# Kernel optimization log

Measured on AMD Instinct MI355X. Metric: run time of the kernel, lower is better.

The kernel has to match this reference:

```python
import math
import jax, jax.numpy as jnp
import numpy as np
from jax import lax

B, S, D, H, L, F, V = 4, 2048, 768, 12, 6, 3072, 512
HD = D // H
EPS = 1e-5


def setup_inputs():
    key = jax.random.key(0)
    ks = jax.random.split(key, 18)
    std = 0.02
    inp = {
        'x': jax.random.randint(ks[0], (B, S), 0, V, dtype=jnp.int64)
            if jax.config.jax_enable_x64 else jax.random.randint(ks[0], (B, S), 0, V, dtype=jnp.int32),
        'emb': jax.random.normal(ks[1], (V, D), jnp.float32) * std,
        'qkv_w': jax.random.normal(ks[2], (L, D, 3 * D), jnp.float32) * std,
        'qkv_b': jnp.zeros((L, 3 * D), jnp.float32),
        'out_w': jax.random.normal(ks[3], (L, D, D), jnp.float32) * std,
        'out_b': jnp.zeros((L, D), jnp.float32),
        'ln1_s': jnp.ones((L, D), jnp.float32),
        'ln1_b': jnp.zeros((L, D), jnp.float32),
        'w1': jax.random.normal(ks[4], (L, D, F), jnp.float32) * std,
        'b1': jnp.zeros((L, F), jnp.float32),
        'w2': jax.random.normal(ks[5], (L, F, D), jnp.float32) * std,
        'b2': jnp.zeros((L, D), jnp.float32),
        'ln2_s': jnp.ones((L, D), jnp.float32),
        'ln2_b': jnp.zeros((L, D), jnp.float32),
        'lnf_s': jnp.ones((D,), jnp.float32),
        'lnf_b': jnp.zeros((D,), jnp.float32),
        'head_w': jax.random.normal(ks[6], (D, V), jnp.float32) * std,
        'head_b': jnp.zeros((V,), jnp.float32),
    }
    return inp


def _layer_norm(x, s, b):
    mu = jnp.mean(x, -1, keepdims=True)
    var = jnp.mean(jnp.square(x - mu), -1, keepdims=True)
    return (x - mu) * lax.rsqrt(var + EPS) * s + b


def _pos_encoding(seq_len, d_model, dtype):
    pos = jnp.arange(seq_len, dtype=dtype)[:, None]
    div = jnp.exp(jnp.arange(0, d_model, 2, dtype=dtype) * (-math.log(10000.0) / d_model))
    pe = jnp.zeros((seq_len, d_model), dtype)
    pe = pe.at[:, 0::2].set(jnp.sin(pos * div))
    pe = pe.at[:, 1::2].set(jnp.cos(pos * div))
    return pe


def reference(x, emb, qkv_w, qkv_b, out_w, out_b, ln1_s, ln1_b,
              w1, b1, w2, b2, ln2_s, ln2_b, lnf_s, lnf_b, head_w, head_b):
    b, s = x.shape
    d = emb.shape[1]
    h = emb[x] * math.sqrt(d)                      # [B,S,D]
    h = h + _pos_encoding(s, d, h.dtype)
    causal = jnp.tril(jnp.ones((s, s), bool))      # [S,S]
    scale = HD ** -0.5

    def block(hcarry, p):
        qw, qb, ow, ob, l1s, l1b, w1i, b1i, w2i, b2i, l2s, l2b = p
        xn = _layer_norm(hcarry, l1s, l1b)
        qkv = xn @ qw + qb                          # [B,S,3D]
        qkv = qkv.reshape(b, s, 3, H, HD).transpose(2, 0, 3, 1, 4)
        q, k, v = qkv[0], qkv[1], qkv[2]            # each [B,H,S,hd]
        scores = jnp.einsum('bhqd,bhkd->bhqk', q, k) * scale
        scores = jnp.where(causal, scores, -jnp.inf)
        attn = jax.nn.softmax(scores, axis=-1)
        o = jnp.einsum('bhqk,bhkd->bhqd', attn, v)
        o = o.transpose(0, 2, 1, 3).reshape(b, s, d)
        hcarry = hcarry + (o @ ow + ob)
        xn2 = _layer_norm(hcarry, l2s, l2b)
        ff = jax.nn.relu(xn2 @ w1i + b1i) @ w2i + b2i
        return hcarry + ff, None

    h, _ = lax.scan(block, h, (qkv_w, qkv_b, out_w, out_b, ln1_s, ln1_b,
                               w1, b1, w2, b2, ln2_s, ln2_b))
    h = _layer_norm(h, lnf_s, lnf_b)
    return h @ head_w + head_b                     # [B,S,V]
```

## Files before the change

kernel.cpp:

```cpp
#include <hip/hip_runtime.h>
#include <math.h>
#include <stdio.h>

#define Bv 4
#define Sv 2048
#define Dv 768
#define Hv 12
#define Lv 6
#define Fv 3072
#define Vv 512
#define Mv (Bv*Sv)

typedef __bf16 bf16;
typedef __bf16 bf16x8 __attribute__((ext_vector_type(8)));
typedef __bf16 bf16x4 __attribute__((ext_vector_type(4)));
typedef short  s16x4  __attribute__((ext_vector_type(4)));
typedef float  f32x4  __attribute__((ext_vector_type(4)));

__device__ __forceinline__ void gload_lds16(const void* g, void* l) {
  __builtin_amdgcn_global_load_lds(
      (__attribute__((address_space(1))) void*)(void*)g,
      (__attribute__((address_space(3))) void*)l, 16, 0, 0);
}

__device__ __forceinline__ int xcd_remap(int orig, int nwg) {
  int q = nwg >> 3, r = nwg & 7;
  int xcd = orig & 7, loc = orig >> 3;
  return (xcd < r ? xcd * (q + 1) : r * (q + 1) + (xcd - r) * q) + loc;
}

__global__ void detect_i64(const int* __restrict__ x, int* __restrict__ flag) {
  __shared__ int red[256];
  int acc = 0;
  for (int i = threadIdx.x; i < Mv / 2; i += 256) acc |= x[2 * i + 1];
  red[threadIdx.x] = acc;
  __syncthreads();
  for (int s = 128; s > 0; s >>= 1) {
    if (threadIdx.x < s) red[threadIdx.x] |= red[threadIdx.x + s];
    __syncthreads();
  }
  if (threadIdx.x == 0) *flag = (red[0] == 0) ? 1 : 0;
}

__global__ void embed_kernel(const int* __restrict__ x, const float* __restrict__ emb,
                             float* __restrict__ h, const int* __restrict__ i64flag) {
  int idx = blockIdx.x * 256 + threadIdx.x;
  int j  = idx % (Dv / 2);
  int bs = idx / (Dv / 2);
  int s  = bs % Sv;
  int tok = (*i64flag) ? x[2 * bs] : x[bs];
  float2 e = *(const float2*)(emb + (size_t)tok * Dv + 2 * j);
  float div = expf((float)(2 * j) * (-9.210340371976184f / (float)Dv));
  float arg = (float)s * div;
  const float sq = 27.712812921102035f;
  float2 o;
  o.x = e.x * sq + sinf(arg);
  o.y = e.y * sq + cosf(arg);
  *(float2*)(h + (size_t)bs * Dv + 2 * j) = o;
}

__global__ void transpose_cvt(const float* __restrict__ in, bf16* __restrict__ out,
                              int K, int N) {
  __shared__ float tile[64][65];
  in  += (size_t)blockIdx.z * K * N;
  out += (size_t)blockIdx.z * K * N;
  int n0 = blockIdx.x * 64, k0 = blockIdx.y * 64;
  int tx = threadIdx.x & 63, ty = threadIdx.x >> 6;
#pragma unroll
  for (int i = 0; i < 64; i += 4)
    tile[ty + i][tx] = in[(size_t)(k0 + ty + i) * N + n0 + tx];
  __syncthreads();
#pragma unroll
  for (int i = 0; i < 64; i += 4)
    out[(size_t)(n0 + ty + i) * K + k0 + tx] = (bf16)tile[tx][ty + i];
}

__global__ void vtrans(const bf16* __restrict__ qkv, bf16* __restrict__ vt) {
  __shared__ bf16 tile[64][72];
  const int st = blockIdx.x;
  const int bh = blockIdx.y;
  const int b = bh / Hv, h = bh % Hv;
  const bf16* src = qkv + ((size_t)b * Sv + st * 64) * 2304 + 1536 + h * 64;
  const int rl = threadIdx.x >> 3;
  const int c8 = (threadIdx.x & 7) * 8;
#pragma unroll
  for (int i = 0; i < 2; ++i) {
    bf16x8 v = *(const bf16x8*)(src + (size_t)(rl + i * 32) * 2304 + c8);
    *(bf16x8*)&tile[rl + i * 32][c8] = v;
  }
  __syncthreads();
  bf16* dst = vt + ((size_t)bh * 64) * Sv + st * 64;
#pragma unroll
  for (int i = 0; i < 2; ++i) {
    bf16 tmp[8];
#pragma unroll
    for (int j = 0; j < 8; ++j) tmp[j] = tile[c8 + j][rl + i * 32];
    *(bf16x8*)(dst + (size_t)(rl + i * 32) * Sv + c8) = *(bf16x8*)tmp;
  }
}

__global__ void ln_kernel(const float* __restrict__ hin, const float* __restrict__ sc,
                          const float* __restrict__ bi, bf16* __restrict__ out) {
  int row  = blockIdx.x * 4 + (threadIdx.x >> 6);
  int lane = threadIdx.x & 63;
  const float* p = hin + (size_t)row * Dv + lane * 12;
  float v[12];
  *(float4*)(v)     = *(const float4*)(p);
  *(float4*)(v + 4) = *(const float4*)(p + 4);
  *(float4*)(v + 8) = *(const float4*)(p + 8);
  float sum = 0.f, sq = 0.f;
#pragma unroll
  for (int j = 0; j < 12; ++j) { sum += v[j]; sq += v[j] * v[j]; }
#pragma unroll
  for (int m = 1; m < 64; m <<= 1) {
    sum += __shfl_xor(sum, m, 64);
    sq  += __shfl_xor(sq,  m, 64);
  }
  float mu  = sum * (1.f / 768.f);
  float var = sq * (1.f / 768.f) - mu * mu;
  float rs  = rsqrtf(var + 1e-5f);
  float s_[12], b_[12];
  const float* scp = sc + lane * 12;
  const float* bip = bi + lane * 12;
  *(float4*)(s_)     = *(const float4*)(scp);
  *(float4*)(s_ + 4) = *(const float4*)(scp + 4);
  *(float4*)(s_ + 8) = *(const float4*)(scp + 8);
  *(float4*)(b_)     = *(const float4*)(bip);
  *(float4*)(b_ + 4) = *(const float4*)(bip + 4);
  *(float4*)(b_ + 8) = *(const float4*)(bip + 8);
  union { bf16 h2[12]; uint2 q[3]; } ob;
#pragma unroll
  for (int j = 0; j < 12; ++j)
    ob.h2[j] = (bf16)((v[j] - mu) * rs * s_[j] + b_[j]);
  uint2* op = (uint2*)(out + (size_t)row * Dv + lane * 12);
  op[0] = ob.q[0]; op[1] = ob.q[1]; op[2] = ob.q[2];
}

template<bool RELU, bool RESID, int OUTMODE>
__global__ __launch_bounds__(256) void gemm_bt(
    const bf16* __restrict__ A, const bf16* __restrict__ Bt,
    const float* __restrict__ bias, float* __restrict__ hres,
    bf16* __restrict__ outb, float* __restrict__ outf, int M, int N, int K) {
  __shared__ bf16 sA[2][128 * 64];
  __shared__ bf16 sB[2][128 * 64];
  const int gx = gridDim.x;
  const int wg = xcd_remap(blockIdx.y * gx + blockIdx.x, gx * gridDim.y);
  const int bn = (wg % gx) * 128, bm = (wg / gx) * 128;
  const int t = threadIdx.x, lane = t & 63, wid = t >> 6;
  const int wr = wid >> 1, wc = wid & 1;
  const int g = lane >> 4, c = lane & 15;
  f32x4 acc[4][4];
#pragma unroll
  for (int i = 0; i < 4; ++i)
#pragma unroll
    for (int j = 0; j < 4; ++j) acc[i][j] = (f32x4){0.f, 0.f, 0.f, 0.f};
  const int nkt = K >> 6;

  auto stage = [&](int bb, int kt) {
#pragma unroll
    for (int j2 = 0; j2 < 4; ++j2) {
      int ch  = t + j2 * 256;
      int row = ch >> 3;
      int src = ((ch & 7) * 8) ^ ((row & 7) << 3);
      gload_lds16(A  + (size_t)(bm + row) * K + kt * 64 + src, &sA[bb][ch * 8]);
      gload_lds16(Bt + (size_t)(bn + row) * K + kt * 64 + src, &sB[bb][ch * 8]);
    }
  };

  stage(0, 0);
  const int swz = (c & 7) << 3;
  for (int kt = 0; kt < nkt; ++kt) {
    const int cb = kt & 1;
    if (kt + 1 < nkt) {
      stage(cb ^ 1, kt + 1);
      asm volatile("s_waitcnt vmcnt(8)" ::: "memory");
    } else {
      asm volatile("s_waitcnt vmcnt(0)" ::: "memory");
    }
    __builtin_amdgcn_s_barrier();
    __builtin_amdgcn_sched_barrier(0);
#pragma unroll
    for (int f = 0; f < 2; ++f) {
      bf16x8 aF[4], bF[4];
      const int e = (f * 32 + g * 8) ^ swz;
#pragma unroll
      for (int mt = 0; mt < 4; ++mt)
        aF[mt] = *(const bf16x8*)&sA[cb][(wr * 64 + mt * 16 + c) * 64 + e];
#pragma unroll
      for (int nt = 0; nt < 4; ++nt)
        bF[nt] = *(const bf16x8*)&sB[cb][(wc * 64 + nt * 16 + c) * 64 + e];
      __builtin_amdgcn_s_setprio(1);
#pragma unroll
      for (int mt = 0; mt < 4; ++mt)
#pragma unroll
        for (int nt = 0; nt < 4; ++nt)
          acc[mt][nt] = __builtin_amdgcn_mfma_f32_16x16x32_bf16(
              aF[mt], bF[nt], acc[mt][nt], 0, 0, 0);
      __builtin_amdgcn_s_setprio(0);
    }
    __builtin_amdgcn_sched_barrier(0);
    __builtin_amdgcn_s_barrier();
  }
#pragma unroll
  for (int nt = 0; nt < 4; ++nt) {
    int col = bn + wc * 64 + nt * 16 + c;
    float bv = bias[col];
#pragma unroll
    for (int mt = 0; mt < 4; ++mt) {
      int row0 = bm + wr * 64 + mt * 16 + g * 4;
#pragma unroll
      for (int r = 0; r < 4; ++r) {
        float vv = acc[mt][nt][r] + bv;
        if (RELU) vv = fmaxf(vv, 0.f);
        size_t off = (size_t)(row0 + r) * N + col;
        if (RESID) { vv += hres[off]; hres[off] = vv; }
        if (OUTMODE == 1) outb[off] = (bf16)vv;
        if (OUTMODE == 2) outf[off] = vv;
      }
    }
  }
}

template<bool RELU, bool RESID, int OUTMODE>
__global__ __launch_bounds__(256) void gemm_sk(
    const bf16* __restrict__ A, const bf16* __restrict__ Bt,
    const float* __restrict__ bias, float* __restrict__ hres,
    bf16* __restrict__ outb, float* __restrict__ outf, int M, int N, int K) {
  __shared__ bf16 sA[2][64 * 64];
  __shared__ bf16 sB[2][128 * 64];
  const int gx = gridDim.x;
  const int wg = xcd_remap(blockIdx.y * gx + blockIdx.x, gx * gridDim.y);
  const int bn = (wg % gx) * 128, bm = (wg / gx) * 64;
  const int t = threadIdx.x, lane = t & 63, wid = t >> 6;
  const int wr = wid >> 1, wc = wid & 1;
  const int g = lane >> 4, c = lane & 15;
  f32x4 acc[2][4];
#pragma unroll
  for (int i = 0; i < 2; ++i)
#pragma unroll
    for (int j = 0; j < 4; ++j) acc[i][j] = (f32x4){0.f, 0.f, 0.f, 0.f};
  const int nkt = K >> 6;

  auto stage = [&](int bb, int kt) {
#pragma unroll
    for (int j2 = 0; j2 < 2; ++j2) {
      int ch  = t + j2 * 256;
      int row = ch >> 3;
      int src = ((ch & 7) * 8) ^ ((row & 7) << 3);
      gload_lds16(A + (size_t)(bm + row) * K + kt * 64 + src, &sA[bb][ch * 8]);
    }
#pragma unroll
    for (int j2 = 0; j2 < 4; ++j2) {
      int ch  = t + j2 * 256;
      int row = ch >> 3;
      int src = ((ch & 7) * 8) ^ ((row & 7) << 3);
      gload_lds16(Bt + (size_t)(bn + row) * K + kt * 64 + src, &sB[bb][ch * 8]);
    }
  };

  stage(0, 0);
  const int swz = (c & 7) << 3;
  for (int kt = 0; kt < nkt; ++kt) {
    const int cb = kt & 1;
    if (kt + 1 < nkt) {
      stage(cb ^ 1, kt + 1);
      asm volatile("s_waitcnt vmcnt(6)" ::: "memory");
    } else {
      asm volatile("s_waitcnt vmcnt(0)" ::: "memory");
    }
    __builtin_amdgcn_s_barrier();
    __builtin_amdgcn_sched_barrier(0);
#pragma unroll
    for (int f = 0; f < 2; ++f) {
      bf16x8 aF[2], bF[4];
      const int e = (f * 32 + g * 8) ^ swz;
#pragma unroll
      for (int mt = 0; mt < 2; ++mt)
        aF[mt] = *(const bf16x8*)&sA[cb][(wr * 32 + mt * 16 + c) * 64 + e];
#pragma unroll
      for (int nt = 0; nt < 4; ++nt)
        bF[nt] = *(const bf16x8*)&sB[cb][(wc * 64 + nt * 16 + c) * 64 + e];
      __builtin_amdgcn_s_setprio(1);
#pragma unroll
      for (int mt = 0; mt < 2; ++mt)
#pragma unroll
        for (int nt = 0; nt < 4; ++nt)
          acc[mt][nt] = __builtin_amdgcn_mfma_f32_16x16x32_bf16(
              aF[mt], bF[nt], acc[mt][nt], 0, 0, 0);
      __builtin_amdgcn_s_setprio(0);
    }
    __builtin_amdgcn_sched_barrier(0);
    __builtin_amdgcn_s_barrier();
  }
#pragma unroll
  for (int nt = 0; nt < 4; ++nt) {
    int col = bn + wc * 64 + nt * 16 + c;
    float bv = bias[col];
#pragma unroll
    for (int mt = 0; mt < 2; ++mt) {
      int row0 = bm + wr * 32 + mt * 16 + g * 4;
#pragma unroll
      for (int r = 0; r < 4; ++r) {
        float vv = acc[mt][nt][r] + bv;
        if (RELU) vv = fmaxf(vv, 0.f);
        size_t off = (size_t)(row0 + r) * N + col;
        if (RESID) { vv += hres[off]; hres[off] = vv; }
        if (OUTMODE == 1) outb[off] = (bf16)vv;
        if (OUTMODE == 2) outf[off] = vv;
      }
    }
  }
}

__global__ __launch_bounds__(256) void attn_kernel(const bf16* __restrict__ qkv,
                                                   const bf16* __restrict__ vt,
                                                   bf16* __restrict__ o) {
  __shared__ bf16 sK[2][64 * 64], sVT[2][64 * 64];
  const int nwg = 16 * Bv * Hv;
  const int wgl = xcd_remap(blockIdx.y * 16 + blockIdx.x, nwg);
  const int i  = wgl % 16;
  const int bh = wgl / 16;
  const int qtA = i, qtB = 31 - i;
  const int b  = bh / Hv;
  const int h  = bh % Hv;
  const int t = threadIdx.x, lane = t & 63, wid = t >> 6;
  const int g = lane >> 4, c = lane & 15;
  const int QST = 2304;
  const bf16* qbase  = qkv + (size_t)b * Sv * QST + h * 64;
  const bf16* vtbase = vt + ((size_t)bh * 64) * Sv;
  const float CS = 0.18033688011112042f;
  const float THR = 11.541560327111707f;
  const int swz = (c & 7) << 3;
  const s16x4 onesf = {0x3F80, 0x3F80, 0x3F80, 0x3F80};

  bf16x8 qfA[2], qfB[2];
  {
    const bf16* qa = qbase + (size_t)(qtA * 64 + wid * 16 + c) * QST;
    qfA[0] = *(const bf16x8*)(qa + g * 8);
    qfA[1] = *(const bf16x8*)(qa + 32 + g * 8);
    const bf16* qb = qbase + (size_t)(qtB * 64 + wid * 16 + c) * QST;
    qfB[0] = *(const bf16x8*)(qb + g * 8);
    qfB[1] = *(const bf16x8*)(qb + 32 + g * 8);
  }
  f32x4 accA[4], accB[4];
  f32x4 accLA = {0.f, 0.f, 0.f, 0.f}, accLB = {0.f, 0.f, 0.f, 0.f};
  float mA = -INFINITY, mB = -INFINITY;
#pragma unroll
  for (int d0 = 0; d0 < 4; ++d0) {
    accA[d0] = (f32x4){0.f, 0.f, 0.f, 0.f};
    accB[d0] = (f32x4){0.f, 0.f, 0.f, 0.f};
  }
  const int qlA = qtA * 64 + wid * 16 + c;
  const int qlB = qtB * 64 + wid * 16 + c;

  auto stage = [&](int bb, int kt) {
#pragma unroll
    for (int j2 = 0; j2 < 2; ++j2) {
      int ch  = t + j2 * 256;
      int row = ch >> 3;
      int src = ((ch & 7) * 8) ^ ((row & 7) << 3);
      gload_lds16(qbase + (size_t)(kt * 64 + row) * QST + 768 + src, &sK[bb][ch * 8]);
      gload_lds16(vtbase + (size_t)row * Sv + kt * 64 + src, &sVT[bb][ch * 8]);
    }
  };

  auto process = [&](int bb, const bf16x8* qf, f32x4* accO, f32x4& accL,
                     float& m_s, int ql, int kt, bool diag) {
    f32x4 accT[4];
#pragma unroll
    for (int nt = 0; nt < 4; ++nt) accT[nt] = (f32x4){0.f, 0.f, 0.f, 0.f};
    __builtin_amdgcn_s_setprio(1);
#pragma unroll
    for (int nt = 0; nt < 4; ++nt)
#pragma unroll
      for (int f = 0; f < 2; ++f) {
        bf16x8 kf = *(const bf16x8*)&sK[bb][(nt * 16 + c) * 64 + ((f * 32 + g * 8) ^ swz)];
        accT[nt] = __builtin_amdgcn_mfma_f32_16x16x32_bf16(kf, qf[f], accT[nt], 0, 0, 0);
      }
    __builtin_amdgcn_s_setprio(0);
    if (diag) {
#pragma unroll
      for (int nt = 0; nt < 4; ++nt)
#pragma unroll
        for (int r = 0; r < 4; ++r)
          if ((kt * 64 + nt * 16 + g * 4 + r) > ql) accT[nt][r] = -INFINITY;
    }
    float mt = -INFINITY;
#pragma unroll
    for (int nt = 0; nt < 4; ++nt)
#pragma unroll
      for (int r = 0; r < 4; ++r) mt = fmaxf(mt, accT[nt][r]);
    mt *= CS;
    mt = fmaxf(mt, __shfl_xor(mt, 16, 64));
    mt = fmaxf(mt, __shfl_xor(mt, 32, 64));
    const bool skip = __all(mt <= m_s + THR);
    const float mn = skip ? m_s : fmaxf(m_s, mt);
    if (!skip) {
      float al = __builtin_amdgcn_exp2f(m_s - mn);
      m_s = mn;
#pragma unroll
      for (int r = 0; r < 4; ++r) {
        float alq = __shfl(al, g * 4 + r, 64);
        accL[r] *= alq;
#pragma unroll
        for (int d0 = 0; d0 < 4; ++d0) accO[d0][r] *= alq;
      }
    }
#pragma unroll
    for (int nt = 0; nt < 4; ++nt)
#pragma unroll
      for (int r = 0; r < 4; ++r)
        accT[nt][r] = __builtin_amdgcn_exp2f(fmaf(accT[nt][r], CS, -mn));
    s16x4 pa[4];
#pragma unroll
    for (int nt = 0; nt < 4; ++nt) {
      bf16x4 pb;
#pragma unroll
      for (int r = 0; r < 4; ++r) pb[r] = (bf16)accT[nt][r];
      pa[nt] = __builtin_bit_cast(s16x4, pb);
    }
    __builtin_amdgcn_s_setprio(1);
#pragma unroll
    for (int nt = 0; nt < 4; ++nt)
      accL = __builtin_amdgcn_mfma_f32_16x16x16bf16_1k(pa[nt], onesf, accL, 0, 0, 0);
#pragma unroll
    for (int d0 = 0; d0 < 4; ++d0) {
      const int drow = (d0 * 16 + c) * 64;
#pragma unroll
      for (int nt = 0; nt < 4; ++nt) {
        int chunk = (nt * 2 + (g >> 1)) ^ (c & 7);
        s16x4 vfr = *(const s16x4*)&sVT[bb][drow + chunk * 8 + (g & 1) * 4];
        accO[d0] = __builtin_amdgcn_mfma_f32_16x16x16bf16_1k(pa[nt], vfr, accO[d0], 0, 0, 0);
      }
    }
    __builtin_amdgcn_s_setprio(0);
  };

  stage(0, 0);
  int cur = 0;
  for (int kt = 0; kt <= qtB; ++kt) {
    __syncthreads();
    if (kt < qtB) stage(cur ^ 1, kt + 1);
    if (kt <= qtA) process(cur, qfA, accA, accLA, mA, qlA, kt, kt == qtA);
    process(cur, qfB, accB, accLB, mB, qlB, kt, kt == qtB);
    cur ^= 1;
  }

#pragma unroll
  for (int r = 0; r < 4; ++r) {
    float iA = 1.f / accLA[r];
    float iB = 1.f / accLB[r];
    size_t orA = (size_t)b * Sv + qtA * 64 + wid * 16 + g * 4 + r;
    size_t orB = (size_t)b * Sv + qtB * 64 + wid * 16 + g * 4 + r;
#pragma unroll
    for (int d0 = 0; d0 < 4; ++d0) {
      o[orA * Dv + h * 64 + d0 * 16 + c] = (bf16)(accA[d0][r] * iA);
      o[orB * Dv + h * 64 + d0 * 16 + c] = (bf16)(accB[d0][r] * iB);
    }
  }
}

extern "C" void kernel_launch(void* const* d_in, const int* in_sizes, int n_in,
                              void* d_out, int out_size, void* d_ws, size_t ws_size,
                              hipStream_t stream) {
  const int*   x     = (const int*)d_in[0];
  const float* emb   = (const float*)d_in[1];
  const float* qkv_w = (const float*)d_in[2];
  const float* qkv_b = (const float*)d_in[3];
  const float* out_w = (const float*)d_in[4];
  const float* out_b = (const float*)d_in[5];
  const float* ln1_s = (const float*)d_in[6];
  const float* ln1_b = (const float*)d_in[7];
  const float* w1    = (const float*)d_in[8];
  const float* b1    = (const float*)d_in[9];
  const float* w2    = (const float*)d_in[10];
  const float* b2    = (const float*)d_in[11];
  const float* ln2_s = (const float*)d_in[12];
  const float* ln2_b = (const float*)d_in[13];
  const float* lnf_s = (const float*)d_in[14];
  const float* lnf_b = (const float*)d_in[15];
  const float* head_w= (const float*)d_in[16];
  const float* head_b= (const float*)d_in[17];
  float* out = (float*)d_out;
  (void)in_sizes; (void)n_in; (void)out_size;

  char* ws = (char*)d_ws;
  size_t off = 0;
  auto alloc = [&](size_t bytes) -> char* {
    char* p = ws + off; off += (bytes + 255) & ~(size_t)255; return p;
  };
  float* hbuf  = (float*)alloc((size_t)Mv * Dv * 4);
  bf16*  xn    = (bf16*) alloc((size_t)Mv * Dv * 2);
  bf16*  qkvff = (bf16*) alloc((size_t)Mv * Fv * 2);
  bf16*  vt    = (bf16*) alloc((size_t)Bv * Hv * 64 * Sv * 2);
  bf16*  attn_o= (bf16*) alloc((size_t)Mv * Dv * 2);
  bf16*  qkvT  = (bf16*) alloc((size_t)Lv * 3 * Dv * Dv * 2);
  bf16*  outT  = (bf16*) alloc((size_t)Lv * Dv * Dv * 2);
  bf16*  w1T   = (bf16*) alloc((size_t)Lv * Fv * Dv * 2);
  bf16*  w2T   = (bf16*) alloc((size_t)Lv * Fv * Dv * 2);
  bf16*  headT = (bf16*) alloc((size_t)Vv * Dv * 2);
  int*   i64f  = (int*)  alloc(256);

  fprintf(stderr, "[kernel_launch] ws_size=%zu needed=%zu out_size=%d\n",
          ws_size, off, out_size);
  if (off > ws_size) {
    fprintf(stderr, "[kernel_launch] WORKSPACE TOO SMALL - not launching\n");
    return;
  }

  detect_i64<<<1, 256, 0, stream>>>(x, i64f);
  transpose_cvt<<<dim3(36, 12, Lv), 256, 0, stream>>>(qkv_w, qkvT, Dv, 3 * Dv);
  transpose_cvt<<<dim3(12, 12, Lv), 256, 0, stream>>>(out_w, outT, Dv, Dv);
  transpose_cvt<<<dim3(48, 12, Lv), 256, 0, stream>>>(w1, w1T, Dv, Fv);
  transpose_cvt<<<dim3(12, 48, Lv), 256, 0, stream>>>(w2, w2T, Fv, Dv);
  transpose_cvt<<<dim3(8, 12, 1), 256, 0, stream>>>(head_w, headT, Dv, Vv);
  embed_kernel<<<Mv * (Dv / 2) / 256, 256, 0, stream>>>(x, emb, hbuf, i64f);

  for (int l = 0; l < Lv; ++l) {
    ln_kernel<<<Mv / 4, 256, 0, stream>>>(hbuf, ln1_s + l * Dv, ln1_b + l * Dv, xn);
    gemm_bt<false, false, 1><<<dim3(3 * Dv / 128, Mv / 128), 256, 0, stream>>>(
        xn, qkvT + (size_t)l * 3 * Dv * Dv, qkv_b + l * 3 * Dv, nullptr, qkvff,
        nullptr, Mv, 3 * Dv, Dv);
    vtrans<<<dim3(Sv / 64, Bv * Hv), 256, 0, stream>>>(qkvff, vt);
    attn_kernel<<<dim3(16, Bv * Hv), 256, 0, stream>>>(qkvff, vt, attn_o);
    gemm_sk<false, true, 0><<<dim3(Dv / 128, Mv / 64), 256, 0, stream>>>(
        attn_o, outT + (size_t)l * Dv * Dv, out_b + l * Dv, hbuf, nullptr,
        nullptr, Mv, Dv, Dv);
    ln_kernel<<<Mv / 4, 256, 0, stream>>>(hbuf, ln2_s + l * Dv, ln2_b + l * Dv, xn);
    gemm_bt<true, false, 1><<<dim3(Fv / 128, Mv / 128), 256, 0, stream>>>(
        xn, w1T + (size_t)l * Fv * Dv, b1 + l * Fv, nullptr, qkvff, nullptr,
        Mv, Fv, Dv);
    gemm_sk<false, true, 0><<<dim3(Dv / 128, Mv / 64), 256, 0, stream>>>(
        qkvff, w2T + (size_t)l * Fv * Dv, b2 + l * Dv, hbuf, nullptr, nullptr,
        Mv, Dv, Fv);
  }
  ln_kernel<<<Mv / 4, 256, 0, stream>>>(hbuf, lnf_s, lnf_b, xn);
  gemm_sk<false, false, 2><<<dim3(Vv / 128, Mv / 64), 256, 0, stream>>>(
      xn, headT, head_b, nullptr, nullptr, out, Mv, Vv, Dv);
}
```

Measured before the change: 1.609 ms.

## Fuse V transpose into QKV GEMM epilogue via LDS-staged write

```diff
diff --git a/kernel.cpp b/kernel.cpp
--- a/kernel.cpp
+++ b/kernel.cpp
@@ -75,30 +75,6 @@
     out[(size_t)(n0 + ty + i) * K + k0 + tx] = (bf16)tile[tx][ty + i];
 }
 
-__global__ void vtrans(const bf16* __restrict__ qkv, bf16* __restrict__ vt) {
-  __shared__ bf16 tile[64][72];
-  const int st = blockIdx.x;
-  const int bh = blockIdx.y;
-  const int b = bh / Hv, h = bh % Hv;
-  const bf16* src = qkv + ((size_t)b * Sv + st * 64) * 2304 + 1536 + h * 64;
-  const int rl = threadIdx.x >> 3;
-  const int c8 = (threadIdx.x & 7) * 8;
-#pragma unroll
-  for (int i = 0; i < 2; ++i) {
-    bf16x8 v = *(const bf16x8*)(src + (size_t)(rl + i * 32) * 2304 + c8);
-    *(bf16x8*)&tile[rl + i * 32][c8] = v;
-  }
-  __syncthreads();
-  bf16* dst = vt + ((size_t)bh * 64) * Sv + st * 64;
-#pragma unroll
-  for (int i = 0; i < 2; ++i) {
-    bf16 tmp[8];
-#pragma unroll
-    for (int j = 0; j < 8; ++j) tmp[j] = tile[c8 + j][rl + i * 32];
-    *(bf16x8*)(dst + (size_t)(rl + i * 32) * Sv + c8) = *(bf16x8*)tmp;
-  }
-}
-
 __global__ void ln_kernel(const float* __restrict__ hin, const float* __restrict__ sc,
                           const float* __restrict__ bi, bf16* __restrict__ out) {
   int row  = blockIdx.x * 4 + (threadIdx.x >> 6);
@@ -140,9 +116,9 @@
 __global__ __launch_bounds__(256) void gemm_bt(
     const bf16* __restrict__ A, const bf16* __restrict__ Bt,
     const float* __restrict__ bias, float* __restrict__ hres,
-    bf16* __restrict__ outb, float* __restrict__ outf, int M, int N, int K) {
-  __shared__ bf16 sA[2][128 * 64];
-  __shared__ bf16 sB[2][128 * 64];
+    bf16* __restrict__ outb, float* __restrict__ outf, bf16* __restrict__ vt,
+    int M, int N, int K) {
+  __shared__ bf16 smem[4][128 * 64];
   const int gx = gridDim.x;
   const int wg = xcd_remap(blockIdx.y * gx + blockIdx.x, gx * gridDim.y);
   const int bn = (wg % gx) * 128, bm = (wg / gx) * 128;
@@ -162,8 +138,8 @@
       int ch  = t + j2 * 256;
       int row = ch >> 3;
       int src = ((ch & 7) * 8) ^ ((row & 7) << 3);
-      gload_lds16(A  + (size_t)(bm + row) * K + kt * 64 + src, &sA[bb][ch * 8]);
-      gload_lds16(Bt + (size_t)(bn + row) * K + kt * 64 + src, &sB[bb][ch * 8]);
+      gload_lds16(A  + (size_t)(bm + row) * K + kt * 64 + src, &smem[bb][ch * 8]);
+      gload_lds16(Bt + (size_t)(bn + row) * K + kt * 64 + src, &smem[2 + bb][ch * 8]);
     }
   };
 
@@ -185,10 +161,10 @@
       const int e = (f * 32 + g * 8) ^ swz;
 #pragma unroll
       for (int mt = 0; mt < 4; ++mt)
-        aF[mt] = *(const bf16x8*)&sA[cb][(wr * 64 + mt * 16 + c) * 64 + e];
+        aF[mt] = *(const bf16x8*)&smem[cb][(wr * 64 + mt * 16 + c) * 64 + e];
 #pragma unroll
       for (int nt = 0; nt < 4; ++nt)
-        bF[nt] = *(const bf16x8*)&sB[cb][(wc * 64 + nt * 16 + c) * 64 + e];
+        bF[nt] = *(const bf16x8*)&smem[2 + cb][(wc * 64 + nt * 16 + c) * 64 + e];
       __builtin_amdgcn_s_setprio(1);
 #pragma unroll
       for (int mt = 0; mt < 4; ++mt)
@@ -200,6 +176,36 @@
     }
     __builtin_amdgcn_sched_barrier(0);
     __builtin_amdgcn_s_barrier();
+  }
+  if (OUTMODE == 3 && bn >= 1536) {
+    bf16* ldsT = (bf16*)smem;
+#pragma unroll
+    for (int nt = 0; nt < 4; ++nt) {
+      int lc = wc * 64 + nt * 16 + c;
+      float bv = bias[bn + lc];
+#pragma unroll
+      for (int mt = 0; mt < 4; ++mt) {
+        int lr = wr * 64 + mt * 16 + g * 4;
+        bf16x4 pb;
+#pragma unroll
+        for (int r = 0; r < 4; ++r) pb[r] = (bf16)(acc[mt][nt][r] + bv);
+        *(s16x4*)&ldsT[lc * 136 + lr] = __builtin_bit_cast(s16x4, pb);
+      }
+    }
+    __syncthreads();
+    const int vc0 = bn - 1536;
+    const int bb_ = bm >> 11;
+    const int s0  = bm & 2047;
+#pragma unroll
+    for (int it = 0; it < 8; ++it) {
+      int chunk = t + it * 256;
+      int d = chunk >> 4, sc = chunk & 15;
+      bf16x8 v = *(const bf16x8*)&ldsT[d * 136 + sc * 8];
+      int vcol = vc0 + d;
+      size_t vrow = ((size_t)(bb_ * Hv + (vcol >> 6)) * 64 + (vcol & 63));
+      *(bf16x8*)&vt[vrow * Sv + s0 + sc * 8] = v;
+    }
+    return;
   }
 #pragma unroll
   for (int nt = 0; nt < 4; ++nt) {
@@ -214,7 +220,7 @@
         if (RELU) vv = fmaxf(vv, 0.f);
         size_t off = (size_t)(row0 + r) * N + col;
         if (RESID) { vv += hres[off]; hres[off] = vv; }
-        if (OUTMODE == 1) outb[off] = (bf16)vv;
+        if (OUTMODE == 1 || OUTMODE == 3) outb[off] = (bf16)vv;
         if (OUTMODE == 2) outf[off] = vv;
       }
     }
@@ -385,11 +391,12 @@
         for (int r = 0; r < 4; ++r)
           if ((kt * 64 + nt * 16 + g * 4 + r) > ql) accT[nt][r] = -INFINITY;
     }
-    float mt = -INFINITY;
+    float mnt[4];
 #pragma unroll
     for (int nt = 0; nt < 4; ++nt)
-#pragma unroll
-      for (int r = 0; r < 4; ++r) mt = fmaxf(mt, accT[nt][r]);
+      mnt[nt] = fmaxf(fmaxf(accT[nt][0], accT[nt][1]),
+                      fmaxf(accT[nt][2], accT[nt][3]));
+    float mt = fmaxf(fmaxf(mnt[0], mnt[1]), fmaxf(mnt[2], mnt[3]));
     mt *= CS;
     mt = fmaxf(mt, __shfl_xor(mt, 16, 64));
     mt = fmaxf(mt, __shfl_xor(mt, 32, 64));
@@ -518,10 +525,9 @@
 
   for (int l = 0; l < Lv; ++l) {
     ln_kernel<<<Mv / 4, 256, 0, stream>>>(hbuf, ln1_s + l * Dv, ln1_b + l * Dv, xn);
-    gemm_bt<false, false, 1><<<dim3(3 * Dv / 128, Mv / 128), 256, 0, stream>>>(
+    gemm_bt<false, false, 3><<<dim3(3 * Dv / 128, Mv / 128), 256, 0, stream>>>(
         xn, qkvT + (size_t)l * 3 * Dv * Dv, qkv_b + l * 3 * Dv, nullptr, qkvff,
-        nullptr, Mv, 3 * Dv, Dv);
-    vtrans<<<dim3(Sv / 64, Bv * Hv), 256, 0, stream>>>(qkvff, vt);
+        nullptr, vt, Mv, 3 * Dv, Dv);
     attn_kernel<<<dim3(16, Bv * Hv), 256, 0, stream>>>(qkvff, vt, attn_o);
     gemm_sk<false, true, 0><<<dim3(Dv / 128, Mv / 64), 256, 0, stream>>>(
         attn_o, outT + (size_t)l * Dv * Dv, out_b + l * Dv, hbuf, nullptr,
@@ -529,7 +535,7 @@
     ln_kernel<<<Mv / 4, 256, 0, stream>>>(hbuf, ln2_s + l * Dv, ln2_b + l * Dv, xn);
     gemm_bt<true, false, 1><<<dim3(Fv / 128, Mv / 128), 256, 0, stream>>>(
         xn, w1T + (size_t)l * Fv * Dv, b1 + l * Fv, nullptr, qkvff, nullptr,
-        Mv, Fv, Dv);
+        nullptr, Mv, Fv, Dv);
     gemm_sk<false, true, 0><<<dim3(Dv / 128, Mv / 64), 256, 0, stream>>>(
         qkvff, w2T + (size_t)l * Fv * Dv, b2 + l * Dv, hbuf, nullptr, nullptr,
         Mv, Dv, Fv);
```

Measured after the change: 1.546 ms. -3.9%, faster.
